# Kernel optimization log

Hardware: AMD Instinct MI355X
Metric: run time of the kernel (lower is better)

The kernel has to match this reference:

```python
import jax, jax.numpy as jnp
import numpy as np

B, N, D = 8, 360, 128  # batch, roi_num, input_dim


def setup_inputs() -> dict:
    key = jax.random.key(0)
    k1, k2, k3 = jax.random.split(key, 3)
    embeddings = jax.random.normal(k1, (B, N, D), dtype=jnp.float32)
    # feature_proj: Linear(2D -> D); edge_predictor: Linear(D -> 1)
    W1 = jax.random.normal(k2, (D, 2 * D), dtype=jnp.float32) * (1.0 / np.sqrt(2 * D))
    b1 = jnp.zeros((D,), dtype=jnp.float32)
    W2 = jax.random.normal(k3, (1, D), dtype=jnp.float32) * (1.0 / np.sqrt(D))
    b2 = jnp.zeros((1,), dtype=jnp.float32)
    return {"embeddings": embeddings, "W1": W1, "b1": b1, "W2": W2, "b2": b2}


def reference(embeddings, W1, b1, W2, b2):
    # One-hot matmuls rel_rec @ emb / rel_send @ emb are exact gathers:
    # for edge e = i*N + j: receiver = emb[:, i], sender = emb[:, j].
    b, n, d = embeddings.shape
    senders = jnp.broadcast_to(embeddings[:, None, :, :], (b, n, n, d))    # emb[b, j]
    receivers = jnp.broadcast_to(embeddings[:, :, None, :], (b, n, n, d))  # emb[b, i]
    edge_features = jnp.concatenate([senders, receivers], axis=-1)         # [B,N,N,2D]
    h = jax.nn.relu(jnp.einsum('bijf,df->bijd', edge_features, W1) + b1)   # [B,N,N,D]
    scores = jax.nn.relu(jnp.einsum('bijd,od->bijo', h, W2) + b2)          # [B,N,N,1]
    return scores
```

## Files before the change

### kernel.cpp

```cpp
#include <hip/hip_runtime.h>

#define Bc 8
#define Nc 360
#define Dc 128
#define LDST 132

__global__ __launch_bounds__(256) void proj_kernel(
    const float* __restrict__ emb, const float* __restrict__ W1,
    const float* __restrict__ b1, const float* __restrict__ W2,
    float* __restrict__ Av, float* __restrict__ Bv)
{
    __shared__ float E_s[64 * LDST];
    __shared__ float W_s[32 * Dc];

    const int t  = threadIdx.x;
    const int r0 = blockIdx.x * 64;
    const int c0 = blockIdx.y * 32;
    const bool recv = (c0 >= Dc);
    const int  cl0  = recv ? (c0 - Dc) : c0;
    const int  off  = recv ? Dc : 0;

    const int rsub = t >> 5, c4 = (t & 31) * 4;
    #pragma unroll
    for (int p = 0; p < 8; ++p) {
        const int r = p * 8 + rsub;
        *(float4*)&E_s[r * LDST + c4] = *(const float4*)&emb[(r0 + r) * Dc + c4];
    }
    #pragma unroll
    for (int p = 0; p < 4; ++p) {
        const int r = p * 8 + rsub;
        *(float4*)&W_s[r * Dc + c4] = *(const float4*)&W1[(cl0 + r) * (2 * Dc) + off + c4];
    }
    __syncthreads();

    const int lane = t & 63;
    const int wu   = __builtin_amdgcn_readfirstlane(t >> 6);

    float acc[8];
    #pragma unroll
    for (int cc = 0; cc < 8; ++cc) acc[cc] = 0.0f;

    #pragma unroll 4
    for (int k4 = 0; k4 < 32; ++k4) {
        const float4 e = *(const float4*)&E_s[lane * LDST + k4 * 4];
        #pragma unroll
        for (int cc = 0; cc < 8; ++cc) {
            const float4 wv = *(const float4*)&W_s[(wu * 8 + cc) * Dc + k4 * 4];
            acc[cc] = fmaf(wv.x, e.x, acc[cc]);
            acc[cc] = fmaf(wv.y, e.y, acc[cc]);
            acc[cc] = fmaf(wv.z, e.z, acc[cc]);
            acc[cc] = fmaf(wv.w, e.w, acc[cc]);
        }
    }

    float* dst = (recv ? Av : Bv) + (r0 + lane) * Dc + cl0 + wu * 8;
    #pragma unroll
    for (int cc = 0; cc < 8; ++cc) {
        const int c = cl0 + wu * 8 + cc;
        float v = recv ? (acc[cc] + b1[c]) : acc[cc];
        acc[cc] = v * W2[c];
    }
    #pragma unroll
    for (int q = 0; q < 2; ++q)
        ((float4*)dst)[q] = make_float4(acc[q*4+0], acc[q*4+1], acc[q*4+2], acc[q*4+3]);
}

__global__ __launch_bounds__(256) void edge_kernel(
    const float* __restrict__ Av, const float* __restrict__ Bv,
    const float* __restrict__ W2, const float* __restrict__ b2,
    float* __restrict__ out)
{
    __shared__ float B_s[64 * LDST];
    __shared__ float A_s[36 * LDST];
    __shared__ float s_s[Dc];
    __shared__ float sig_s[64];
    __shared__ float rho_s[36];

    const int t  = threadIdx.x;
    const int b  = blockIdx.z;
    const int j0 = blockIdx.x * 64;
    const int i0 = blockIdx.y * 36;

    const int rsub = t >> 5, c4 = (t & 31) * 4;
    #pragma unroll
    for (int p = 0; p < 8; ++p) {
        const int r = p * 8 + rsub;
        int jr = j0 + r; if (jr > Nc - 1) jr = Nc - 1;
        *(float4*)&B_s[r * LDST + c4] = *(const float4*)&Bv[(b * Nc + jr) * Dc + c4];
    }
    #pragma unroll
    for (int p = 0; p < 4; ++p) {
        const int r = p * 8 + rsub;
        *(float4*)&A_s[r * LDST + c4] = *(const float4*)&Av[(b * Nc + i0 + r) * Dc + c4];
    }
    if (rsub < 4) {
        const int r = 32 + rsub;
        *(float4*)&A_s[r * LDST + c4] = *(const float4*)&Av[(b * Nc + i0 + r) * Dc + c4];
    }
    __syncthreads();

    const int lane = t & 63;
    const int w    = t >> 6;
    if (w == 0) {
        float4 s = make_float4(0.f, 0.f, 0.f, 0.f);
        #pragma unroll 8
        for (int k4 = 0; k4 < 32; ++k4) {
            const float4 v = *(const float4*)&B_s[lane * LDST + k4 * 4];
            s.x += v.x; s.y += v.y; s.z += v.z; s.w += v.w;
        }
        sig_s[lane] = 0.5f * ((s.x + s.y) + (s.z + s.w));
    } else if (w == 1) {
        if (lane < 36) {
            float4 s = make_float4(0.f, 0.f, 0.f, 0.f);
            #pragma unroll 8
            for (int k4 = 0; k4 < 32; ++k4) {
                const float4 v = *(const float4*)&A_s[lane * LDST + k4 * 4];
                s.x += v.x; s.y += v.y; s.z += v.z; s.w += v.w;
            }
            rho_s[lane] = 0.5f * ((s.x + s.y) + (s.z + s.w));
        }
    } else if (w == 2) {
        s_s[lane] = copysignf(0.5f, W2[lane]);
    } else {
        s_s[64 + lane] = copysignf(0.5f, W2[64 + lane]);
    }
    __syncthreads();

    const int wu = __builtin_amdgcn_readfirstlane(w);
    float acc[9];
    #pragma unroll
    for (int q = 0; q < 9; ++q) acc[q] = 0.0f;

    #pragma unroll 4
    for (int k4 = 0; k4 < 32; ++k4) {
        const float4 bv = *(const float4*)&B_s[lane * LDST + k4 * 4];
        const float4 sv = *(const float4*)&s_s[k4 * 4];
        #pragma unroll
        for (int q = 0; q < 9; ++q) {
            const float4 av = *(const float4*)&A_s[(wu * 9 + q) * LDST + k4 * 4];
            const float t0 = av.x + bv.x;
            const float t1 = av.y + bv.y;
            const float t2 = av.z + bv.z;
            const float t3 = av.w + bv.w;
            acc[q] = fmaf(sv.x, fabsf(t0), acc[q]);
            acc[q] = fmaf(sv.y, fabsf(t1), acc[q]);
            acc[q] = fmaf(sv.z, fabsf(t2), acc[q]);
            acc[q] = fmaf(sv.w, fabsf(t3), acc[q]);
        }
    }

    const int jg = j0 + lane;
    if (jg < Nc) {
        const float base = b2[0] + sig_s[lane];
        #pragma unroll
        for (int q = 0; q < 9; ++q) {
            const int ig = i0 + wu * 9 + q;
            out[(b * Nc + ig) * Nc + jg] = fmaxf(base + rho_s[wu * 9 + q] + acc[q], 0.0f);
        }
    }
}

extern "C" void kernel_launch(void* const* d_in, const int* in_sizes, int n_in,
                              void* d_out, int out_size, void* d_ws, size_t ws_size,
                              hipStream_t stream) {
    const float* emb = (const float*)d_in[0];
    const float* W1  = (const float*)d_in[1];
    const float* b1  = (const float*)d_in[2];
    const float* W2  = (const float*)d_in[3];
    const float* b2  = (const float*)d_in[4];
    float* out = (float*)d_out;

    float* Av = (float*)d_ws;
    float* Bv = Av + Bc * Nc * Dc;

    proj_kernel<<<dim3(Bc * Nc / 64, 8), 256, 0, stream>>>(emb, W1, b1, W2, Av, Bv);
    edge_kernel<<<dim3(6, 10, Bc), 256, 0, stream>>>(Av, Bv, W2, b2, out);
}
```

Measured before the change: 37.09 us.

## Stream wave-uniform operands via scalar loads and precompute row sums in projection

Both kernels now read wave-uniform operands (W1 rows in the projection, A rows and sign vector in the edge kernel) through inline-asm scalar loads into SGPRs instead of staging them in LDS. Per-row sums of A and B and the sign vector are computed once in the projection kernel via atomics, which removes the LDS reduction pass and one barrier from the edge kernel. The edge tile shrinks to 24 rows per block for a larger grid. It adds a memset launch and float atomics, and each loop iteration waits for its scalar loads to complete with no overlap.

New measurement: 67.29 us. 1.81x slower.

```diff
diff --git a/kernel.cpp b/kernel.cpp
--- a/kernel.cpp
+++ b/kernel.cpp
@@ -5,157 +5,176 @@
 #define Dc 128
 #define LDST 132
 
+typedef float f32x4 __attribute__((ext_vector_type(4)));
+
+__device__ __forceinline__ const float* uptr(const float* p) {
+    unsigned long long v = (unsigned long long)p;
+    unsigned lo = __builtin_amdgcn_readfirstlane((unsigned)(v & 0xffffffffu));
+    unsigned hi = __builtin_amdgcn_readfirstlane((unsigned)(v >> 32));
+    return (const float*)((((unsigned long long)hi) << 32) | lo);
+}
+
+__device__ __forceinline__ void sload_w8(const float* base,
+    f32x4& A0, f32x4& A1, f32x4& A2, f32x4& A3,
+    f32x4& A4, f32x4& A5, f32x4& A6, f32x4& A7)
+{
+    asm volatile(
+        "s_load_dwordx4 %0, %8, 0x0\n\t"
+        "s_load_dwordx4 %1, %8, 0x400\n\t"
+        "s_load_dwordx4 %2, %8, 0x800\n\t"
+        "s_load_dwordx4 %3, %8, 0xc00\n\t"
+        "s_load_dwordx4 %4, %8, 0x1000\n\t"
+        "s_load_dwordx4 %5, %8, 0x1400\n\t"
+        "s_load_dwordx4 %6, %8, 0x1800\n\t"
+        "s_load_dwordx4 %7, %8, 0x1c00\n\t"
+        "s_waitcnt lgkmcnt(0)"
+        : "=&s"(A0), "=&s"(A1), "=&s"(A2), "=&s"(A3),
+          "=&s"(A4), "=&s"(A5), "=&s"(A6), "=&s"(A7)
+        : "s"(base)
+        : "memory");
+}
+
+__device__ __forceinline__ void sload_a6s(const float* abase, const float* sbase,
+    f32x4& A0, f32x4& A1, f32x4& A2, f32x4& A3, f32x4& A4, f32x4& A5, f32x4& Sv)
+{
+    asm volatile(
+        "s_load_dwordx4 %0, %7, 0x0\n\t"
+        "s_load_dwordx4 %1, %7, 0x200\n\t"
+        "s_load_dwordx4 %2, %7, 0x400\n\t"
+        "s_load_dwordx4 %3, %7, 0x600\n\t"
+        "s_load_dwordx4 %4, %7, 0x800\n\t"
+        "s_load_dwordx4 %5, %7, 0xa00\n\t"
+        "s_load_dwordx4 %6, %8, 0x0\n\t"
+        "s_waitcnt lgkmcnt(0)"
+        : "=&s"(A0), "=&s"(A1), "=&s"(A2), "=&s"(A3), "=&s"(A4), "=&s"(A5), "=&s"(Sv)
+        : "s"(abase), "s"(sbase)
+        : "memory");
+}
+
 __global__ __launch_bounds__(256) void proj_kernel(
     const float* __restrict__ emb, const float* __restrict__ W1,
     const float* __restrict__ b1, const float* __restrict__ W2,
-    float* __restrict__ Av, float* __restrict__ Bv)
+    float* __restrict__ Av, float* __restrict__ Bv, float* __restrict__ s_arr,
+    float* __restrict__ rsA, float* __restrict__ rsB)
 {
     __shared__ float E_s[64 * LDST];
-    __shared__ float W_s[32 * Dc];
-
     const int t  = threadIdx.x;
     const int r0 = blockIdx.x * 64;
-    const int c0 = blockIdx.y * 32;
-    const bool recv = (c0 >= Dc);
-    const int  cl0  = recv ? (c0 - Dc) : c0;
-    const int  off  = recv ? Dc : 0;
-
-    const int rsub = t >> 5, c4 = (t & 31) * 4;
-    #pragma unroll
-    for (int p = 0; p < 8; ++p) {
-        const int r = p * 8 + rsub;
-        *(float4*)&E_s[r * LDST + c4] = *(const float4*)&emb[(r0 + r) * Dc + c4];
-    }
-    #pragma unroll
-    for (int p = 0; p < 4; ++p) {
-        const int r = p * 8 + rsub;
-        *(float4*)&W_s[r * Dc + c4] = *(const float4*)&W1[(cl0 + r) * (2 * Dc) + off + c4];
+
+    if (blockIdx.x == 0 && blockIdx.y == 0 && t < Dc)
+        s_arr[t] = copysignf(0.5f, W2[t]);
+
+    {
+        const int rsub = t >> 5, c4 = (t & 31) * 4;
+        #pragma unroll
+        for (int p = 0; p < 8; ++p) {
+            const int r = p * 8 + rsub;
+            *(float4*)&E_s[r * LDST + c4] = *(const float4*)&emb[(r0 + r) * Dc + c4];
+        }
     }
     __syncthreads();
 
     const int lane = t & 63;
     const int wu   = __builtin_amdgcn_readfirstlane(t >> 6);
+    const int c0   = blockIdx.y * 32 + wu * 8;
+    const bool recv = (c0 >= Dc);
+    const int  cl   = recv ? (c0 - Dc) : c0;
+    const float* wbase = uptr(W1 + cl * (2 * Dc) + (recv ? Dc : 0));
 
     float acc[8];
     #pragma unroll
     for (int cc = 0; cc < 8; ++cc) acc[cc] = 0.0f;
 
-    #pragma unroll 4
+    #pragma unroll
     for (int k4 = 0; k4 < 32; ++k4) {
-        const float4 e = *(const float4*)&E_s[lane * LDST + k4 * 4];
+        f32x4 Wv[8];
+        sload_w8(wbase, Wv[0], Wv[1], Wv[2], Wv[3], Wv[4], Wv[5], Wv[6], Wv[7]);
+        const f32x4 ev = *(const f32x4*)&E_s[lane * LDST + k4 * 4];
         #pragma unroll
         for (int cc = 0; cc < 8; ++cc) {
-            const float4 wv = *(const float4*)&W_s[(wu * 8 + cc) * Dc + k4 * 4];
-            acc[cc] = fmaf(wv.x, e.x, acc[cc]);
-            acc[cc] = fmaf(wv.y, e.y, acc[cc]);
-            acc[cc] = fmaf(wv.z, e.z, acc[cc]);
-            acc[cc] = fmaf(wv.w, e.w, acc[cc]);
-        }
-    }
-
-    float* dst = (recv ? Av : Bv) + (r0 + lane) * Dc + cl0 + wu * 8;
+            acc[cc] = fmaf(Wv[cc][0], ev[0], acc[cc]);
+            acc[cc] = fmaf(Wv[cc][1], ev[1], acc[cc]);
+            acc[cc] = fmaf(Wv[cc][2], ev[2], acc[cc]);
+            acc[cc] = fmaf(Wv[cc][3], ev[3], acc[cc]);
+        }
+        wbase += 4;
+    }
+
     #pragma unroll
     for (int cc = 0; cc < 8; ++cc) {
-        const int c = cl0 + wu * 8 + cc;
-        float v = recv ? (acc[cc] + b1[c]) : acc[cc];
-        acc[cc] = v * W2[c];
-    }
-    #pragma unroll
-    for (int q = 0; q < 2; ++q)
-        ((float4*)dst)[q] = make_float4(acc[q*4+0], acc[q*4+1], acc[q*4+2], acc[q*4+3]);
+        float v = recv ? (acc[cc] + b1[cl + cc]) : acc[cc];
+        acc[cc] = v * W2[cl + cc];
+    }
+    float* dst = (recv ? Av : Bv) + (r0 + lane) * Dc + cl;
+    *(float4*)(dst + 0) = make_float4(acc[0], acc[1], acc[2], acc[3]);
+    *(float4*)(dst + 4) = make_float4(acc[4], acc[5], acc[6], acc[7]);
+
+    const float sum8 = ((acc[0] + acc[1]) + (acc[2] + acc[3]))
+                     + ((acc[4] + acc[5]) + (acc[6] + acc[7]));
+    atomicAdd((recv ? rsA : rsB) + (r0 + lane), sum8);
 }
 
 __global__ __launch_bounds__(256) void edge_kernel(
     const float* __restrict__ Av, const float* __restrict__ Bv,
-    const float* __restrict__ W2, const float* __restrict__ b2,
+    const float* __restrict__ s_arr, const float* __restrict__ b2,
+    const float* __restrict__ rsA, const float* __restrict__ rsB,
     float* __restrict__ out)
 {
     __shared__ float B_s[64 * LDST];
-    __shared__ float A_s[36 * LDST];
-    __shared__ float s_s[Dc];
-    __shared__ float sig_s[64];
-    __shared__ float rho_s[36];
-
     const int t  = threadIdx.x;
     const int b  = blockIdx.z;
     const int j0 = blockIdx.x * 64;
-    const int i0 = blockIdx.y * 36;
-
-    const int rsub = t >> 5, c4 = (t & 31) * 4;
-    #pragma unroll
-    for (int p = 0; p < 8; ++p) {
-        const int r = p * 8 + rsub;
-        int jr = j0 + r; if (jr > Nc - 1) jr = Nc - 1;
-        *(float4*)&B_s[r * LDST + c4] = *(const float4*)&Bv[(b * Nc + jr) * Dc + c4];
-    }
-    #pragma unroll
-    for (int p = 0; p < 4; ++p) {
-        const int r = p * 8 + rsub;
-        *(float4*)&A_s[r * LDST + c4] = *(const float4*)&Av[(b * Nc + i0 + r) * Dc + c4];
-    }
-    if (rsub < 4) {
-        const int r = 32 + rsub;
-        *(float4*)&A_s[r * LDST + c4] = *(const float4*)&Av[(b * Nc + i0 + r) * Dc + c4];
+    const int i0 = blockIdx.y * 24;
+
+    {
+        const int rsub = t >> 5, c4 = (t & 31) * 4;
+        #pragma unroll
+        for (int p = 0; p < 8; ++p) {
+            const int r = p * 8 + rsub;
+            int jr = j0 + r; if (jr > Nc - 1) jr = Nc - 1;
+            *(float4*)&B_s[r * LDST + c4] = *(const float4*)&Bv[(b * Nc + jr) * Dc + c4];
+        }
     }
     __syncthreads();
 
     const int lane = t & 63;
-    const int w    = t >> 6;
-    if (w == 0) {
-        float4 s = make_float4(0.f, 0.f, 0.f, 0.f);
-        #pragma unroll 8
-        for (int k4 = 0; k4 < 32; ++k4) {
-            const float4 v = *(const float4*)&B_s[lane * LDST + k4 * 4];
-            s.x += v.x; s.y += v.y; s.z += v.z; s.w += v.w;
-        }
-        sig_s[lane] = 0.5f * ((s.x + s.y) + (s.z + s.w));
-    } else if (w == 1) {
-        if (lane < 36) {
-            float4 s = make_float4(0.f, 0.f, 0.f, 0.f);
-            #pragma unroll 8
-            for (int k4 = 0; k4 < 32; ++k4) {
-                const float4 v = *(const float4*)&A_s[lane * LDST + k4 * 4];
-                s.x += v.x; s.y += v.y; s.z += v.z; s.w += v.w;
+    const int wu   = __builtin_amdgcn_readfirstlane(t >> 6);
+    const int ia   = i0 + wu * 6;
+    const float* ap = uptr(Av + (b * Nc + ia) * Dc);
+    const float* sp = uptr(s_arr);
+
+    float acc[6];
+    #pragma unroll
+    for (int q = 0; q < 6; ++q) acc[q] = 0.0f;
+
+    #pragma unroll
+    for (int k4 = 0; k4 < 32; ++k4) {
+        f32x4 A[6], Sv;
+        sload_a6s(ap, sp, A[0], A[1], A[2], A[3], A[4], A[5], Sv);
+        const f32x4 bv = *(const f32x4*)&B_s[lane * LDST + k4 * 4];
+        #pragma unroll
+        for (int e = 0; e < 4; ++e) {
+            const float se = Sv[e];
+            const float be = bv[e];
+            #pragma unroll
+            for (int q = 0; q < 6; ++q) {
+                const float tq = A[q][e] + be;
+                acc[q] = fmaf(se, fabsf(tq), acc[q]);
             }
-            rho_s[lane] = 0.5f * ((s.x + s.y) + (s.z + s.w));
-        }
-    } else if (w == 2) {
-        s_s[lane] = copysignf(0.5f, W2[lane]);
-    } else {
-        s_s[64 + lane] = copysignf(0.5f, W2[64 + lane]);
-    }
-    __syncthreads();
-
-    const int wu = __builtin_amdgcn_readfirstlane(w);
-    float acc[9];
-    #pragma unroll
-    for (int q = 0; q < 9; ++q) acc[q] = 0.0f;
-
-    #pragma unroll 4
-    for (int k4 = 0; k4 < 32; ++k4) {
-        const float4 bv = *(const float4*)&B_s[lane * LDST + k4 * 4];
-        const float4 sv = *(const float4*)&s_s[k4 * 4];
-        #pragma unroll
-        for (int q = 0; q < 9; ++q) {
-            const float4 av = *(const float4*)&A_s[(wu * 9 + q) * LDST + k4 * 4];
-            const float t0 = av.x + bv.x;
-            const float t1 = av.y + bv.y;
-            const float t2 = av.z + bv.z;
-            const float t3 = av.w + bv.w;
-            acc[q] = fmaf(sv.x, fabsf(t0), acc[q]);
-            acc[q] = fmaf(sv.y, fabsf(t1), acc[q]);
-            acc[q] = fmaf(sv.z, fabsf(t2), acc[q]);
-            acc[q] = fmaf(sv.w, fabsf(t3), acc[q]);
-        }
+        }
+        ap += 4; sp += 4;
     }
 
     const int jg = j0 + lane;
+    const int jc = jg > Nc - 1 ? Nc - 1 : jg;
+    const float sigj = rsB[b * Nc + jc];
     if (jg < Nc) {
-        const float base = b2[0] + sig_s[lane];
-        #pragma unroll
-        for (int q = 0; q < 9; ++q) {
-            const int ig = i0 + wu * 9 + q;
-            out[(b * Nc + ig) * Nc + jg] = fmaxf(base + rho_s[wu * 9 + q] + acc[q], 0.0f);
+        const float bb = b2[0];
+        #pragma unroll
+        for (int q = 0; q < 6; ++q) {
+            const float rho = rsA[b * Nc + ia + q];
+            out[(b * Nc + ia + q) * Nc + jg] =
+                fmaxf(fmaf(0.5f, rho + sigj, acc[q]) + bb, 0.0f);
         }
     }
 }
@@ -170,9 +189,13 @@
     const float* b2  = (const float*)d_in[4];
     float* out = (float*)d_out;
 
-    float* Av = (float*)d_ws;
-    float* Bv = Av + Bc * Nc * Dc;
-
-    proj_kernel<<<dim3(Bc * Nc / 64, 8), 256, 0, stream>>>(emb, W1, b1, W2, Av, Bv);
-    edge_kernel<<<dim3(6, 10, Bc), 256, 0, stream>>>(Av, Bv, W2, b2, out);
-}
+    float* Av    = (float*)d_ws;
+    float* Bv    = Av + Bc * Nc * Dc;
+    float* s_arr = Bv + Bc * Nc * Dc;
+    float* rsA   = s_arr + Dc;
+    float* rsB   = rsA + Bc * Nc;
+
+    hipMemsetAsync(rsA, 0, 2 * Bc * Nc * sizeof(float), stream);
+    proj_kernel<<<dim3(Bc * Nc / 64, 8), 256, 0, stream>>>(emb, W1, b1, W2, Av, Bv, s_arr, rsA, rsB);
+    edge_kernel<<<dim3(6, 15, Bc), 256, 0, stream>>>(Av, Bv, s_arr, b2, rsA, rsB, out);
+}
```
